# Optimization experiments

Hardware: AMD Instinct MI355X
Metric: run time of the kernel (lower is better)

## Reference

```python
import jax, jax.numpy as jnp
import numpy as np

N = 50000      # nodes
E = 800000     # edges
C = 128        # feature width (in = hidden = out)
H = 2          # attention heads
ATT_SLOPE = 0.2   # GATConv leaky_relu slope
OUT_SLOPE = 0.01  # F.leaky_relu_ default slope


def setup_inputs() -> dict:
    key = jax.random.key(0)
    ks = jax.random.split(key, 12)
    s = 1.0 / np.sqrt(C)
    inp = {
        "x": jax.random.normal(ks[0], (N, C), jnp.float32),
        "edge_index": jax.random.randint(ks[1], (2, E), 0, N, dtype=jnp.int32),
        "edge_attr": jax.random.normal(ks[2], (E, C), jnp.float32),
        # GATConv layer 1 params (lin weight, att_src, att_dst, bias)
        "W1": jax.random.normal(ks[3], (C, H * C), jnp.float32) * s,
        "a_src1": jax.random.normal(ks[4], (H, C), jnp.float32) * s,
        "a_dst1": jax.random.normal(ks[5], (H, C), jnp.float32) * s,
        "b1": jnp.zeros((C,), jnp.float32),
        # GATConv layer 2 params
        "W2": jax.random.normal(ks[6], (C, H * C), jnp.float32) * s,
        "a_src2": jax.random.normal(ks[7], (H, C), jnp.float32) * s,
        "a_dst2": jax.random.normal(ks[8], (H, C), jnp.float32) * s,
        "b2": jnp.zeros((C,), jnp.float32),
    }
    return inp


def _segment_softmax(alpha, dst, n):
    # alpha: [E', H]; softmax over edges sharing the same dst node
    amax = jax.ops.segment_max(alpha, dst, num_segments=n)
    amax = jnp.where(jnp.isfinite(amax), amax, 0.0)
    ex = jnp.exp(alpha - amax[dst])
    denom = jax.ops.segment_sum(ex, dst, num_segments=n)
    return ex / (denom[dst] + 1e-16)


def _gat_layer(x, src, dst, W, a_s, a_d, b):
    # GATConv, concat=False (mean over heads), edge_dim=None, eval mode
    n = x.shape[0]
    xp = (x @ W).reshape(n, H, C)                  # [N,H,C]
    a_i = jnp.sum(xp * a_s, axis=-1)               # [N,H] src scores
    a_j = jnp.sum(xp * a_d, axis=-1)               # [N,H] dst scores
    e = jax.nn.leaky_relu(a_i[src] + a_j[dst], ATT_SLOPE)   # [E',H]
    att = _segment_softmax(e, dst, n)              # [E',H]
    msg = att[:, :, None] * xp[src]                # [E',H,C]
    out = jax.ops.segment_sum(msg, dst, num_segments=n)     # [N,H,C]
    return out.mean(axis=1) + b                    # concat=False -> mean heads


def reference(x, edge_index, edge_attr, W1, a_src1, a_dst1, b1,
              W2, a_src2, a_dst2, b2):
    src0, dst0 = edge_index[0], edge_index[1]
    loop = jnp.arange(x.shape[0], dtype=edge_index.dtype)
    src = jnp.concatenate([src0, loop])            # add self loops
    dst = jnp.concatenate([dst0, loop])
    score = None
    for (W, a_s, a_d, b) in ((W1, a_src1, a_dst1, b1),
                             (W2, a_src2, a_dst2, b2)):
        x = _gat_layer(x, src, dst, W, a_s, a_d, b)
        # edge score uses pre-activation x (leaky_relu_ happens after the gather)
        score = jnp.sum(x[src0] * x[dst0] * edge_attr, axis=-1)  # [E]
        x = jax.nn.leaky_relu(x, OUT_SLOPE)
        score = jax.nn.sigmoid(score)
    return x, score
```

## Files before the change

kernel.cpp:

```cpp
#include <hip/hip_runtime.h>
#include <hip/hip_bf16.h>

#define NN 50000
#define EE 800000
#define CC 128
#define HH 2
#define ATT_SLOPE 0.2f
#define OUT_SLOPE 0.01f

__device__ __forceinline__ float lrelu(float v, float s) {
    return v > 0.0f ? v : s * v;
}


__global__ void zero_kernel(int* __restrict__ p, int n) {
    int i = blockIdx.x * blockDim.x + threadIdx.x;
    if (i < n) p[i] = 0;
}

__global__ void count_kernel(const int* __restrict__ dst, int* __restrict__ cnt,
                             int E, int N) {
    int i = blockIdx.x * blockDim.x + threadIdx.x;
    int total = E + N;
    if (i >= total) return;
    int d = (i < E) ? dst[i] : (i - E);
    atomicAdd(&cnt[d], 1);
}

__global__ __launch_bounds__(256) void bsum_kernel(const int* __restrict__ cnt,
                                                   int* __restrict__ bsum, int n) {
    __shared__ int sh[4];
    int i = blockIdx.x * 256 + threadIdx.x;
    int v = (i < n) ? cnt[i] : 0;
    #pragma unroll
    for (int off = 32; off; off >>= 1) v += __shfl_xor(v, off);
    if ((threadIdx.x & 63) == 0) sh[threadIdx.x >> 6] = v;
    __syncthreads();
    if (threadIdx.x == 0) bsum[blockIdx.x] = sh[0] + sh[1] + sh[2] + sh[3];
}

__global__ __launch_bounds__(256) void bscan_kernel(int* __restrict__ bsum, int nb) {
    __shared__ int buf[2][256];
    int t = threadIdx.x;
    int v = (t < nb) ? bsum[t] : 0;
    buf[0][t] = v;
    __syncthreads();
    int cur = 0;
    for (int off = 1; off < 256; off <<= 1) {
        int nxt = cur ^ 1;
        int add = (t >= off) ? buf[cur][t - off] : 0;
        buf[nxt][t] = buf[cur][t] + add;
        __syncthreads();
        cur = nxt;
    }
    if (t < nb) bsum[t] = buf[cur][t] - v;
}

__global__ __launch_bounds__(256) void scan2_kernel(const int* __restrict__ cnt,
                                                    const int* __restrict__ boff,
                                                    int* __restrict__ rowptr,
                                                    int* __restrict__ fillptr, int n) {
    __shared__ int buf[2][256];
    int t = threadIdx.x;
    int i = blockIdx.x * 256 + t;
    int v = (i < n) ? cnt[i] : 0;
    buf[0][t] = v;
    __syncthreads();
    int cur = 0;
    for (int off = 1; off < 256; off <<= 1) {
        int nxt = cur ^ 1;
        int add = (t >= off) ? buf[cur][t - off] : 0;
        buf[nxt][t] = buf[cur][t] + add;
        __syncthreads();
        cur = nxt;
    }
    int excl = buf[cur][t] - v + boff[blockIdx.x];
    if (i < n) { rowptr[i] = excl; fillptr[i] = excl; }
    if (i == n - 1) rowptr[n] = excl + v;
}

__global__ void scatter_kernel(const int* __restrict__ src, const int* __restrict__ dst,
                               int* __restrict__ fillptr, int* __restrict__ col,
                               int E, int N) {
    int i = blockIdx.x * blockDim.x + threadIdx.x;
    int total = E + N;
    if (i >= total) return;
    int s, d;
    if (i < E) { s = src[i]; d = dst[i]; }
    else       { s = d = i - E; }
    int pos = atomicAdd(&fillptr[d], 1);
    col[pos] = s;
}


__global__ __launch_bounds__(256) void gemm_kernel(const float* __restrict__ X,
                            const float* __restrict__ W,
                            float* __restrict__ XP, int M, float slope) {
    __shared__ float As[64][68];
    __shared__ float Bs[64][64];
    int m0 = blockIdx.x * 64;
    int n0 = blockIdx.y * 64;
    int t  = threadIdx.x;
    int tx = t & 15;
    int ty = t >> 4;

    float acc[4][4] = {};

    for (int kt = 0; kt < 2; ++kt) {
        #pragma unroll
        for (int j = 0; j < 4; ++j) {
            int idx = t + j * 256;
            int row = idx >> 4;
            int kq  = idx & 15;
            float4 v = make_float4(0.f, 0.f, 0.f, 0.f);
            if (m0 + row < M)
                v = *(const float4*)(X + (size_t)(m0 + row) * CC + kt * 64 + kq * 4);
            v.x = lrelu(v.x, slope); v.y = lrelu(v.y, slope);
            v.z = lrelu(v.z, slope); v.w = lrelu(v.w, slope);
            As[row][kq * 4 + 0] = v.x;
            As[row][kq * 4 + 1] = v.y;
            As[row][kq * 4 + 2] = v.z;
            As[row][kq * 4 + 3] = v.w;
        }
        #pragma unroll
        for (int j = 0; j < 4; ++j) {
            int idx = t + j * 256;
            int k   = idx >> 4;
            int cq  = idx & 15;
            *(float4*)(&Bs[k][cq * 4]) =
                *(const float4*)(W + (size_t)(kt * 64 + k) * 256 + n0 + cq * 4);
        }
        __syncthreads();
        #pragma unroll
        for (int k = 0; k < 64; ++k) {
            float a0 = As[ty * 4 + 0][k];
            float a1 = As[ty * 4 + 1][k];
            float a2 = As[ty * 4 + 2][k];
            float a3 = As[ty * 4 + 3][k];
            float4 bv = *(const float4*)(&Bs[k][tx * 4]);
            acc[0][0] += a0 * bv.x; acc[0][1] += a0 * bv.y; acc[0][2] += a0 * bv.z; acc[0][3] += a0 * bv.w;
            acc[1][0] += a1 * bv.x; acc[1][1] += a1 * bv.y; acc[1][2] += a1 * bv.z; acc[1][3] += a1 * bv.w;
            acc[2][0] += a2 * bv.x; acc[2][1] += a2 * bv.y; acc[2][2] += a2 * bv.z; acc[2][3] += a2 * bv.w;
            acc[3][0] += a3 * bv.x; acc[3][1] += a3 * bv.y; acc[3][2] += a3 * bv.z; acc[3][3] += a3 * bv.w;
        }
        __syncthreads();
    }
    #pragma unroll
    for (int i = 0; i < 4; ++i) {
        int row = m0 + ty * 4 + i;
        if (row < M) {
            float4 o = make_float4(acc[i][0], acc[i][1], acc[i][2], acc[i][3]);
            *(float4*)(XP + (size_t)row * 256 + n0 + tx * 4) = o;
        }
    }
}

__global__ __launch_bounds__(256) void a4_kernel(const float* __restrict__ xp,
                          const float* __restrict__ a_src,
                          const float* __restrict__ a_dst,
                          float* __restrict__ a4) {
    int n = blockIdx.x * 4 + (int)(threadIdx.x >> 6);
    int lane = threadIdx.x & 63;
    int h = lane >> 5;
    int c = (lane & 31) * 4;
    float4 xv  = *(const float4*)(xp + (size_t)n * 256 + lane * 4);
    float4 asv = *(const float4*)(a_src + h * 128 + c);
    float4 adv = *(const float4*)(a_dst + h * 128 + c);
    float ss = xv.x * asv.x + xv.y * asv.y + xv.z * asv.z + xv.w * asv.w;
    float sd = xv.x * adv.x + xv.y * adv.y + xv.z * adv.z + xv.w * adv.w;
    #pragma unroll
    for (int off = 16; off; off >>= 1) {
        ss += __shfl_xor(ss, off);
        sd += __shfl_xor(sd, off);
    }
    if ((lane & 31) == 0) {
        a4[n * 4 + h]     = ss;
        a4[n * 4 + 2 + h] = sd;
    }
}

__global__ __launch_bounds__(256) void agg_kernel(const float* __restrict__ xp,
                           const float* __restrict__ a4,
                           const int* __restrict__ rowptr,
                           const int* __restrict__ col,
                           const float* __restrict__ bias,
                           float* __restrict__ out_pre) {
    int n = __builtin_amdgcn_readfirstlane(blockIdx.x * 4 + (int)(threadIdx.x >> 6));
    int lane = threadIdx.x & 63;
    int h = lane >> 5;
    int r0 = rowptr[n], r1 = rowptr[n + 1];
    float2 adv = *(const float2*)(a4 + (size_t)n * 4 + 2);
    float ad = h ? adv.y : adv.x;

    float denom = 0.f;
    float4 acc = make_float4(0.f, 0.f, 0.f, 0.f);

    int k = r0;
    for (; k + 1 < r1; k += 2) {
        int s0 = __builtin_amdgcn_readfirstlane(col[k]);
        int s1 = __builtin_amdgcn_readfirstlane(col[k + 1]);
        float2 av0 = *(const float2*)(a4 + (size_t)s0 * 4);
        float2 av1 = *(const float2*)(a4 + (size_t)s1 * 4);
        float4 v0 = *(const float4*)(xp + (size_t)s0 * 256 + lane * 4);
        float4 v1 = *(const float4*)(xp + (size_t)s1 * 256 + lane * 4);
        float e0 = lrelu((h ? av0.y : av0.x) + ad, ATT_SLOPE);
        float e1 = lrelu((h ? av1.y : av1.x) + ad, ATT_SLOPE);
        float x0 = __expf(e0);
        float x1 = __expf(e1);
        denom += x0 + x1;
        acc.x += x0 * v0.x + x1 * v1.x;
        acc.y += x0 * v0.y + x1 * v1.y;
        acc.z += x0 * v0.z + x1 * v1.z;
        acc.w += x0 * v0.w + x1 * v1.w;
    }
    if (k < r1) {
        int s0 = __builtin_amdgcn_readfirstlane(col[k]);
        float2 av0 = *(const float2*)(a4 + (size_t)s0 * 4);
        float4 v0 = *(const float4*)(xp + (size_t)s0 * 256 + lane * 4);
        float e0 = lrelu((h ? av0.y : av0.x) + ad, ATT_SLOPE);
        float x0 = __expf(e0);
        denom += x0;
        acc.x += x0 * v0.x;
        acc.y += x0 * v0.y;
        acc.z += x0 * v0.z;
        acc.w += x0 * v0.w;
    }

    float inv = 1.0f / (denom + 1e-16f);
    float4 val = make_float4(acc.x * inv, acc.y * inv, acc.z * inv, acc.w * inv);
    float4 other;
    other.x = __shfl_xor(val.x, 32);
    other.y = __shfl_xor(val.y, 32);
    other.z = __shfl_xor(val.z, 32);
    other.w = __shfl_xor(val.w, 32);
    if (h == 0) {
        float4 bv = *(const float4*)(bias + lane * 4);
        float4 o;
        o.x = 0.5f * (val.x + other.x) + bv.x;
        o.y = 0.5f * (val.y + other.y) + bv.y;
        o.z = 0.5f * (val.z + other.z) + bv.z;
        o.w = 0.5f * (val.w + other.w) + bv.w;
        *(float4*)(out_pre + (size_t)n * CC + lane * 4) = o;
    }
}

__global__ __launch_bounds__(256) void score_kernel(const float* __restrict__ x2,
                             const int* __restrict__ src,
                             const int* __restrict__ dst,
                             const float* __restrict__ ea,
                             float* __restrict__ score) {
    int e = blockIdx.x * 8 + (int)(threadIdx.x >> 5);
    int q = threadIdx.x & 31;
    int s = src[e], d = dst[e];
    float4 xs = *(const float4*)(x2 + (size_t)s * CC + q * 4);
    float4 xd = *(const float4*)(x2 + (size_t)d * CC + q * 4);
    float4 ev = *(const float4*)(ea + (size_t)e * CC + q * 4);
    float p = xs.x * xd.x * ev.x + xs.y * xd.y * ev.y +
              xs.z * xd.z * ev.z + xs.w * xd.w * ev.w;
    #pragma unroll
    for (int off = 16; off; off >>= 1) p += __shfl_xor(p, off);
    if (q == 0) score[e] = 1.0f / (1.0f + __expf(-p));
}

__global__ void lrelu_kernel(float* __restrict__ x, int n4) {
    int i = blockIdx.x * blockDim.x + threadIdx.x;
    if (i >= n4) return;
    float4 v = ((float4*)x)[i];
    v.x = lrelu(v.x, OUT_SLOPE); v.y = lrelu(v.y, OUT_SLOPE);
    v.z = lrelu(v.z, OUT_SLOPE); v.w = lrelu(v.w, OUT_SLOPE);
    ((float4*)x)[i] = v;
}

extern "C" void kernel_launch(void* const* d_in, const int* in_sizes, int n_in,
                              void* d_out, int out_size, void* d_ws, size_t ws_size,
                              hipStream_t stream) {
    (void)in_sizes; (void)n_in; (void)out_size; (void)ws_size;
    const float* x       = (const float*)d_in[0];
    const int*   eidx    = (const int*)d_in[1];
    const float* ea      = (const float*)d_in[2];
    const float* W1      = (const float*)d_in[3];
    const float* a_src1  = (const float*)d_in[4];
    const float* a_dst1  = (const float*)d_in[5];
    const float* b1      = (const float*)d_in[6];
    const float* W2      = (const float*)d_in[7];
    const float* a_src2  = (const float*)d_in[8];
    const float* a_dst2  = (const float*)d_in[9];
    const float* b2      = (const float*)d_in[10];

    const int* srcp = eidx;
    const int* dstp = eidx + EE;

    char* ws = (char*)d_ws;
    auto alloc = [&](size_t bytes) {
        char* p = ws;
        ws += (bytes + 255) & ~(size_t)255;
        return p;
    };
    const int NB = (NN + 255) / 256;
    int*   cnt     = (int*)alloc((size_t)NN * 4);
    int*   rowptr  = (int*)alloc((size_t)(NN + 1) * 4);
    int*   fillptr = (int*)alloc((size_t)NN * 4);
    int*   col     = (int*)alloc((size_t)(EE + NN) * 4);
    int*   bsum    = (int*)alloc((size_t)NB * 4);
    float* a4      = (float*)alloc((size_t)NN * 4 * 4);
    float* xp      = (float*)alloc((size_t)NN * 256 * 4);
    float* x1      = (float*)alloc((size_t)NN * CC * 4);

    float* outx = (float*)d_out;
    float* outs = outx + (size_t)NN * CC;

    int total = EE + NN;

    zero_kernel<<<(NN + 255) / 256, 256, 0, stream>>>(cnt, NN);
    count_kernel<<<(total + 255) / 256, 256, 0, stream>>>(dstp, cnt, EE, NN);
    bsum_kernel<<<NB, 256, 0, stream>>>(cnt, bsum, NN);
    bscan_kernel<<<1, 256, 0, stream>>>(bsum, NB);
    scan2_kernel<<<NB, 256, 0, stream>>>(cnt, bsum, rowptr, fillptr, NN);
    scatter_kernel<<<(total + 255) / 256, 256, 0, stream>>>(srcp, dstp, fillptr, col, EE, NN);

    dim3 ggrid((NN + 63) / 64, 4);

    gemm_kernel<<<ggrid, 256, 0, stream>>>(x, W1, xp, NN, 1.0f);
    a4_kernel<<<NN / 4, 256, 0, stream>>>(xp, a_src1, a_dst1, a4);
    agg_kernel<<<NN / 4, 256, 0, stream>>>(xp, a4, rowptr, col, b1, x1);

    gemm_kernel<<<ggrid, 256, 0, stream>>>(x1, W2, xp, NN, OUT_SLOPE);
    a4_kernel<<<NN / 4, 256, 0, stream>>>(xp, a_src2, a_dst2, a4);
    agg_kernel<<<NN / 4, 256, 0, stream>>>(xp, a4, rowptr, col, b2, outx);

    score_kernel<<<EE / 8, 256, 0, stream>>>(outx, srcp, dstp, ea, outs);
    lrelu_kernel<<<((NN * CC / 4) + 255) / 256, 256, 0, stream>>>(outx, NN * CC / 4);
}
```

Baseline: 1.083 ms.

## Fuse attention score computation into GEMM epilogue and widen GEMM/aggregation unrolling

```diff
diff --git a/kernel.cpp b/kernel.cpp
--- a/kernel.cpp
+++ b/kernel.cpp
@@ -93,11 +93,21 @@
 }
 
 
+#define GSTEP(AC, BV) \
+    acc[0][0] += a0.AC * BV.x; acc[0][1] += a0.AC * BV.y; acc[0][2] += a0.AC * BV.z; acc[0][3] += a0.AC * BV.w; \
+    acc[1][0] += a1.AC * BV.x; acc[1][1] += a1.AC * BV.y; acc[1][2] += a1.AC * BV.z; acc[1][3] += a1.AC * BV.w; \
+    acc[2][0] += a2.AC * BV.x; acc[2][1] += a2.AC * BV.y; acc[2][2] += a2.AC * BV.z; acc[2][3] += a2.AC * BV.w; \
+    acc[3][0] += a3.AC * BV.x; acc[3][1] += a3.AC * BV.y; acc[3][2] += a3.AC * BV.z; acc[3][3] += a3.AC * BV.w;
+
 __global__ __launch_bounds__(256) void gemm_kernel(const float* __restrict__ X,
                             const float* __restrict__ W,
-                            float* __restrict__ XP, int M, float slope) {
+                            const float* __restrict__ a_src,
+                            const float* __restrict__ a_dst,
+                            float* __restrict__ XP,
+                            float* __restrict__ a4,
+                            int M, float slope) {
     __shared__ float As[64][68];
-    __shared__ float Bs[64][64];
+    __shared__ float Bs[64][68];
     int m0 = blockIdx.x * 64;
     int n0 = blockIdx.y * 64;
     int t  = threadIdx.x;
@@ -117,10 +127,7 @@
                 v = *(const float4*)(X + (size_t)(m0 + row) * CC + kt * 64 + kq * 4);
             v.x = lrelu(v.x, slope); v.y = lrelu(v.y, slope);
             v.z = lrelu(v.z, slope); v.w = lrelu(v.w, slope);
-            As[row][kq * 4 + 0] = v.x;
-            As[row][kq * 4 + 1] = v.y;
-            As[row][kq * 4 + 2] = v.z;
-            As[row][kq * 4 + 3] = v.w;
+            *(float4*)(&As[row][kq * 4]) = v;
         }
         #pragma unroll
         for (int j = 0; j < 4; ++j) {
@@ -132,50 +139,45 @@
         }
         __syncthreads();
         #pragma unroll
-        for (int k = 0; k < 64; ++k) {
-            float a0 = As[ty * 4 + 0][k];
-            float a1 = As[ty * 4 + 1][k];
-            float a2 = As[ty * 4 + 2][k];
-            float a3 = As[ty * 4 + 3][k];
-            float4 bv = *(const float4*)(&Bs[k][tx * 4]);
-            acc[0][0] += a0 * bv.x; acc[0][1] += a0 * bv.y; acc[0][2] += a0 * bv.z; acc[0][3] += a0 * bv.w;
-            acc[1][0] += a1 * bv.x; acc[1][1] += a1 * bv.y; acc[1][2] += a1 * bv.z; acc[1][3] += a1 * bv.w;
-            acc[2][0] += a2 * bv.x; acc[2][1] += a2 * bv.y; acc[2][2] += a2 * bv.z; acc[2][3] += a2 * bv.w;
-            acc[3][0] += a3 * bv.x; acc[3][1] += a3 * bv.y; acc[3][2] += a3 * bv.z; acc[3][3] += a3 * bv.w;
+        for (int k0 = 0; k0 < 64; k0 += 4) {
+            float4 a0 = *(const float4*)(&As[ty * 4 + 0][k0]);
+            float4 a1 = *(const float4*)(&As[ty * 4 + 1][k0]);
+            float4 a2 = *(const float4*)(&As[ty * 4 + 2][k0]);
+            float4 a3 = *(const float4*)(&As[ty * 4 + 3][k0]);
+            float4 b0 = *(const float4*)(&Bs[k0 + 0][tx * 4]);
+            float4 b1 = *(const float4*)(&Bs[k0 + 1][tx * 4]);
+            float4 b2 = *(const float4*)(&Bs[k0 + 2][tx * 4]);
+            float4 b3 = *(const float4*)(&Bs[k0 + 3][tx * 4]);
+            GSTEP(x, b0);
+            GSTEP(y, b1);
+            GSTEP(z, b2);
+            GSTEP(w, b3);
         }
         __syncthreads();
     }
+
+    int h = n0 >> 7;
+    int coff = (n0 & 127) + tx * 4;
+    float4 asv = *(const float4*)(a_src + h * 128 + coff);
+    float4 adv = *(const float4*)(a_dst + h * 128 + coff);
     #pragma unroll
     for (int i = 0; i < 4; ++i) {
         int row = m0 + ty * 4 + i;
+        float4 o = make_float4(acc[i][0], acc[i][1], acc[i][2], acc[i][3]);
+        float ps = o.x * asv.x + o.y * asv.y + o.z * asv.z + o.w * asv.w;
+        float pd = o.x * adv.x + o.y * adv.y + o.z * adv.z + o.w * adv.w;
+        #pragma unroll
+        for (int off = 1; off < 16; off <<= 1) {
+            ps += __shfl_xor(ps, off);
+            pd += __shfl_xor(pd, off);
+        }
         if (row < M) {
-            float4 o = make_float4(acc[i][0], acc[i][1], acc[i][2], acc[i][3]);
             *(float4*)(XP + (size_t)row * 256 + n0 + tx * 4) = o;
-        }
-    }
-}
-
-__global__ __launch_bounds__(256) void a4_kernel(const float* __restrict__ xp,
-                          const float* __restrict__ a_src,
-                          const float* __restrict__ a_dst,
-                          float* __restrict__ a4) {
-    int n = blockIdx.x * 4 + (int)(threadIdx.x >> 6);
-    int lane = threadIdx.x & 63;
-    int h = lane >> 5;
-    int c = (lane & 31) * 4;
-    float4 xv  = *(const float4*)(xp + (size_t)n * 256 + lane * 4);
-    float4 asv = *(const float4*)(a_src + h * 128 + c);
-    float4 adv = *(const float4*)(a_dst + h * 128 + c);
-    float ss = xv.x * asv.x + xv.y * asv.y + xv.z * asv.z + xv.w * asv.w;
-    float sd = xv.x * adv.x + xv.y * adv.y + xv.z * adv.z + xv.w * adv.w;
-    #pragma unroll
-    for (int off = 16; off; off >>= 1) {
-        ss += __shfl_xor(ss, off);
-        sd += __shfl_xor(sd, off);
-    }
-    if ((lane & 31) == 0) {
-        a4[n * 4 + h]     = ss;
-        a4[n * 4 + 2 + h] = sd;
+            if (tx == 0) {
+                atomicAdd(&a4[(size_t)row * 4 + h], ps);
+                atomicAdd(&a4[(size_t)row * 4 + 2 + h], pd);
+            }
+        }
     }
 }
 
@@ -196,24 +198,34 @@
     float4 acc = make_float4(0.f, 0.f, 0.f, 0.f);
 
     int k = r0;
-    for (; k + 1 < r1; k += 2) {
+    for (; k + 3 < r1; k += 4) {
         int s0 = __builtin_amdgcn_readfirstlane(col[k]);
         int s1 = __builtin_amdgcn_readfirstlane(col[k + 1]);
+        int s2 = __builtin_amdgcn_readfirstlane(col[k + 2]);
+        int s3 = __builtin_amdgcn_readfirstlane(col[k + 3]);
         float2 av0 = *(const float2*)(a4 + (size_t)s0 * 4);
         float2 av1 = *(const float2*)(a4 + (size_t)s1 * 4);
+        float2 av2 = *(const float2*)(a4 + (size_t)s2 * 4);
+        float2 av3 = *(const float2*)(a4 + (size_t)s3 * 4);
         float4 v0 = *(const float4*)(xp + (size_t)s0 * 256 + lane * 4);
         float4 v1 = *(const float4*)(xp + (size_t)s1 * 256 + lane * 4);
+        float4 v2 = *(const float4*)(xp + (size_t)s2 * 256 + lane * 4);
+        float4 v3 = *(const float4*)(xp + (size_t)s3 * 256 + lane * 4);
         float e0 = lrelu((h ? av0.y : av0.x) + ad, ATT_SLOPE);
         float e1 = lrelu((h ? av1.y : av1.x) + ad, ATT_SLOPE);
+        float e2 = lrelu((h ? av2.y : av2.x) + ad, ATT_SLOPE);
+        float e3 = lrelu((h ? av3.y : av3.x) + ad, ATT_SLOPE);
         float x0 = __expf(e0);
         float x1 = __expf(e1);
-        denom += x0 + x1;
-        acc.x += x0 * v0.x + x1 * v1.x;
-        acc.y += x0 * v0.y + x1 * v1.y;
-        acc.z += x0 * v0.z + x1 * v1.z;
-        acc.w += x0 * v0.w + x1 * v1.w;
-    }
-    if (k < r1) {
+        float x2 = __expf(e2);
+        float x3 = __expf(e3);
+        denom += (x0 + x1) + (x2 + x3);
+        acc.x += x0 * v0.x + x1 * v1.x + x2 * v2.x + x3 * v3.x;
+        acc.y += x0 * v0.y + x1 * v1.y + x2 * v2.y + x3 * v3.y;
+        acc.z += x0 * v0.z + x1 * v1.z + x2 * v2.z + x3 * v3.z;
+        acc.w += x0 * v0.w + x1 * v1.w + x2 * v2.w + x3 * v3.w;
+    }
+    for (; k < r1; ++k) {
         int s0 = __builtin_amdgcn_readfirstlane(col[k]);
         float2 av0 = *(const float2*)(a4 + (size_t)s0 * 4);
         float4 v0 = *(const float4*)(xp + (size_t)s0 * 256 + lane * 4);
@@ -312,6 +324,7 @@
     int total = EE + NN;
 
     zero_kernel<<<(NN + 255) / 256, 256, 0, stream>>>(cnt, NN);
+    zero_kernel<<<(NN * 4 + 255) / 256, 256, 0, stream>>>((int*)a4, NN * 4);
     count_kernel<<<(total + 255) / 256, 256, 0, stream>>>(dstp, cnt, EE, NN);
     bsum_kernel<<<NB, 256, 0, stream>>>(cnt, bsum, NN);
     bscan_kernel<<<1, 256, 0, stream>>>(bsum, NB);
@@ -320,12 +333,11 @@
 
     dim3 ggrid((NN + 63) / 64, 4);
 
-    gemm_kernel<<<ggrid, 256, 0, stream>>>(x, W1, xp, NN, 1.0f);
-    a4_kernel<<<NN / 4, 256, 0, stream>>>(xp, a_src1, a_dst1, a4);
+    gemm_kernel<<<ggrid, 256, 0, stream>>>(x, W1, a_src1, a_dst1, xp, a4, NN, 1.0f);
     agg_kernel<<<NN / 4, 256, 0, stream>>>(xp, a4, rowptr, col, b1, x1);
 
-    gemm_kernel<<<ggrid, 256, 0, stream>>>(x1, W2, xp, NN, OUT_SLOPE);
-    a4_kernel<<<NN / 4, 256, 0, stream>>>(xp, a_src2, a_dst2, a4);
+    zero_kernel<<<(NN * 4 + 255) / 256, 256, 0, stream>>>((int*)a4, NN * 4);
+    gemm_kernel<<<ggrid, 256, 0, stream>>>(x1, W2, a_src2, a_dst2, xp, a4, NN, OUT_SLOPE);
     agg_kernel<<<NN / 4, 256, 0, stream>>>(xp, a4, rowptr, col, b2, outx);
 
     score_kernel<<<EE / 8, 256, 0, stream>>>(outx, srcp, dstp, ea, outs);
```

Result: no change. 1.066 ms (-1.6%).
